# Kernel tuning notes

Hardware: AMD Instinct MI355X
Metric: run time of the kernel (lower is better)

Reference implementation:

```python
import jax, jax.numpy as jnp
import numpy as np

M, N, EMB, H, ENC, T = 4096, 256, 64, 128, 128, 100


def _lstm_dir(x, Wih, Whh, b, h0, c0):
    # x: (T, M, E); PyTorch LSTM gate order i, f, g, o
    def step(carry, xt):
        h, c = carry
        g = xt @ Wih + h @ Whh + b
        i, f, gg, o = jnp.split(g, 4, axis=-1)
        c = jax.nn.sigmoid(f) * c + jax.nn.sigmoid(i) * jnp.tanh(gg)
        h = jax.nn.sigmoid(o) * jnp.tanh(c)
        return (h, c), h
    _, hs = jax.lax.scan(step, (h0, c0), x)
    return hs  # (T, M, H)


def setup_inputs() -> dict:
    key = jax.random.key(0)
    ks = jax.random.split(key, 14)
    rn = lambda k, sh, s: jax.random.normal(k, sh, jnp.float32) * s
    return {
        "lane_features": jax.random.normal(ks[0], (M, 600), jnp.float32),
        "obs_encoding": jax.random.normal(ks[1], (N, 128), jnp.float32),
        "embed_W": rn(ks[2], (4, EMB), 0.5),
        "embed_b": jnp.zeros((EMB,), jnp.float32),
        "attn_W": rn(ks[3], (128, 100), 0.09),
        "attn_b": jnp.zeros((100,), jnp.float32),
        "Wih_f": rn(ks[4], (EMB, 4 * H), 0.08),
        "Whh_f": rn(ks[5], (H, 4 * H), 0.08),
        "b_f": jnp.zeros((4 * H,), jnp.float32),
        "Wih_b": rn(ks[6], (EMB, 4 * H), 0.08),
        "Whh_b": rn(ks[7], (H, 4 * H), 0.08),
        "b_b": jnp.zeros((4 * H,), jnp.float32),
        "h0": rn(ks[8], (2, 1, H), 0.1),
        "c0": rn(ks[9], (2, 1, H), 0.1),
        "enc_W": rn(ks[10], (8 * H, ENC), 0.03),
        "enc_b": jnp.zeros((ENC,), jnp.float32),
        "same_obs_mask": jax.random.randint(ks[11], (M, 1), 0, N, jnp.int32),
    }


def reference(lane_features, obs_encoding, embed_W, embed_b, attn_W, attn_b,
              Wih_f, Whh_f, b_f, Wih_b, Whh_b, b_b, h0, c0, enc_W, enc_b,
              same_obs_mask):
    Mloc = lane_features.shape[0]
    E = embed_W.shape[1]
    Hh = Whh_f.shape[0]
    # last 400 features -> 100 timesteps x 4 features, then embed + relu
    feat = lane_features[:, -400:].reshape(Mloc * 100, 4)
    lane_embed = jax.nn.relu(feat @ embed_W + embed_b).reshape(Mloc, 100, E)
    # per-obstacle attention over the 100 lane points
    scores = jax.nn.softmax(jax.nn.relu(obs_encoding @ attn_W + attn_b), axis=1)  # (N, 100)
    # the original per-obs_id scatter loop == a single gather by obstacle id
    att = scores[same_obs_mask[:, 0]]  # (M, 100)
    x = jnp.transpose(lane_embed, (1, 0, 2))  # (T, M, E)
    h0f = jnp.broadcast_to(h0[0], (Mloc, Hh)); c0f = jnp.broadcast_to(c0[0], (Mloc, Hh))
    h0b = jnp.broadcast_to(h0[1], (Mloc, Hh)); c0b = jnp.broadcast_to(c0[1], (Mloc, Hh))
    hs_f = _lstm_dir(x, Wih_f, Whh_f, b_f, h0f, c0f)
    hs_b = _lstm_dir(x[::-1], Wih_b, Whh_b, b_b, h0b, c0b)[::-1]
    ls = jnp.transpose(jnp.concatenate([hs_f, hs_b], axis=-1), (1, 0, 2))  # (M, T, 2H)
    front = ls[:, 0, :]
    back = ls[:, -1, :]
    mx = jnp.max(ls, axis=1)
    attn_states = jnp.sum(ls * att[:, :, None], axis=1)
    out = jnp.concatenate([front, back, mx, attn_states], axis=1)  # (M, 8H)
    return jax.nn.relu(out @ enc_W + enc_b)
```

## Files before the change

### kernel.cpp

```cpp
#include <hip/hip_runtime.h>
#include <hip/hip_bf16.h>

#define MROWS 4096
#define TSTEPS 100
#define EMB 64
#define HID 128
#define GATES 512
#define KTOT 192
#define ROWS_PB 32
#define SROW 200

typedef _Float16 half8 __attribute__((ext_vector_type(8)));
typedef _Float16 half4v __attribute__((ext_vector_type(4)));
typedef float f32x4 __attribute__((ext_vector_type(4)));

#define LOG2E  1.44269504f
#define LOG2E2 2.88539008f

__device__ __forceinline__ float rcpf(float x) { return __builtin_amdgcn_rcpf(x); }
__device__ __forceinline__ float ex2(float x) { return __builtin_amdgcn_exp2f(x); }

__global__ void attn_scores_kernel(const float* __restrict__ obs,
                                   const float* __restrict__ attn_W,
                                   const float* __restrict__ attn_b,
                                   float* __restrict__ scores) {
    const int row = blockIdx.x;
    const int tid = threadIdx.x;
    __shared__ float obs_s[128];
    __shared__ float red[128];

    obs_s[tid] = obs[row * 128 + tid];
    __syncthreads();

    float s = -1e30f;
    if (tid < 100) {
        float a = attn_b[tid];
        #pragma unroll 4
        for (int k = 0; k < 128; k++) a += obs_s[k] * attn_W[k * 100 + tid];
        s = fmaxf(a, 0.f);
    }
    red[tid] = s;
    __syncthreads();
    for (int off = 64; off > 0; off >>= 1) {
        if (tid < off) red[tid] = fmaxf(red[tid], red[tid + off]);
        __syncthreads();
    }
    const float m = red[0];
    __syncthreads();
    const float e = (tid < 100) ? __expf(s - m) : 0.f;
    red[tid] = e;
    __syncthreads();
    for (int off = 64; off > 0; off >>= 1) {
        if (tid < off) red[tid] += red[tid + off];
        __syncthreads();
    }
    const float inv = __fdividef(1.f, red[0]);
    if (tid < 100) scores[row * 100 + tid] = e * inv;
}

__global__ void encw_prep_kernel(const float* __restrict__ enc_W,
                                 _Float16* __restrict__ encWT) {
    __shared__ float tile[64][129];
    const int k0 = blockIdx.x * 64;
    const int tid = threadIdx.x;
    #pragma unroll
    for (int i = 0; i < 32; i++) {
        const int idx = tid + i * 256;
        const int rr = idx >> 7, cc = idx & 127;
        tile[rr][cc] = enc_W[(k0 + rr) * 128 + cc];
    }
    __syncthreads();
    const int c = tid >> 1, hh = tid & 1;
    #pragma unroll
    for (int j = 0; j < 32; j++) {
        encWT[c * 1024 + k0 + hh * 32 + j] = (_Float16)tile[hh * 32 + j][c];
    }
}

__launch_bounds__(512, 2)
__global__ void lstm_kernel(const float* __restrict__ lane_features,
                            const float* __restrict__ embed_W,
                            const float* __restrict__ embed_b,
                            const float* __restrict__ Wih_f,
                            const float* __restrict__ Whh_f,
                            const float* __restrict__ b_f,
                            const float* __restrict__ Wih_b,
                            const float* __restrict__ Whh_b,
                            const float* __restrict__ b_b,
                            const float* __restrict__ h0,
                            const float* __restrict__ c0,
                            const int*   __restrict__ mask,
                            const float* __restrict__ scores,
                            float* __restrict__ out_feat) {
    const int blk = blockIdx.x;
    const int d = blk >> 7;
    const int rowbase = (blk & 127) * ROWS_PB;
    const int tid = threadIdx.x;
    const int wave = tid >> 6;
    const int lane = tid & 63;
    const int lane16 = lane & 15;
    const int quad = lane >> 4;

    const float* Wih = d ? Wih_b : Wih_f;
    const float* Whh = d ? Whh_b : Whh_f;
    const float* bia = d ? b_b : b_f;

    __shared__ __attribute__((aligned(16))) _Float16 panel[2][ROWS_PB][SROW];
    __shared__ float att_s[ROWS_PB][100];

    const int erow = tid >> 4;
    const int cc = (tid & 15) * 4;
    float ew_r[4][4], eb_r[4];
    #pragma unroll
    for (int j = 0; j < 4; j++) {
        #pragma unroll
        for (int jj = 0; jj < 4; jj++) ew_r[j][jj] = embed_W[j * EMB + cc + jj];
    }
    #pragma unroll
    for (int jj = 0; jj < 4; jj++) eb_r[jj] = embed_b[cc + jj];

    {
        const int r = tid >> 4, tcol = tid & 15;
        const int mr = mask[rowbase + r];
        for (int t = tcol; t < 100; t += 16) att_s[r][t] = scores[mr * 100 + t];
    }

    const int unitg = wave * 16 + lane16;
    half8 Bf[24];
    #pragma unroll
    for (int ct = 0; ct < 4; ct++) {
        const float scale = (ct == 2) ? LOG2E2 : LOG2E;
        const int col = ct * 128 + unitg;
        #pragma unroll
        for (int ki = 0; ki < 6; ki++) {
            half8 b;
            #pragma unroll
            for (int j = 0; j < 8; j++) {
                const int kk = ki * 32 + quad * 8 + j;
                const float w = (kk < EMB) ? Wih[kk * GATES + col]
                                           : Whh[(kk - EMB) * GATES + col];
                b[j] = (_Float16)(w * scale);
            }
            Bf[ct * 6 + ki] = b;
        }
    }
    float bgate[4];
    #pragma unroll
    for (int ct = 0; ct < 4; ct++)
        bgate[ct] = bia[ct * 128 + unitg] * ((ct == 2) ? LOG2E2 : LOG2E);

    float cst[8], mx[8], as[8], h0s[8], hl[8];
    const float cinit = c0[d * 128 + unitg];
    #pragma unroll
    for (int p = 0; p < 8; p++) {
        cst[p] = cinit; mx[p] = -1e30f; as[p] = 0.f; h0s[p] = 0.f; hl[p] = 0.f;
    }

    for (int idx = tid; idx < ROWS_PB * HID; idx += 512) {
        const int r = idx >> 7, u = idx & 127;
        panel[0][r][EMB + u] = (_Float16)h0[d * 128 + u];
    }

    {
        const int t0 = d ? (TSTEPS - 1) : 0;
        const float4 fv = *(const float4*)(lane_features + (long)(rowbase + erow) * 600 + 200 + 4 * t0);
        #pragma unroll
        for (int jj = 0; jj < 4; jj++) {
            float e = eb_r[jj] + fv.x * ew_r[0][jj] + fv.y * ew_r[1][jj]
                               + fv.z * ew_r[2][jj] + fv.w * ew_r[3][jj];
            panel[0][erow][cc + jj] = (_Float16)fmaxf(e, 0.f);
        }
    }
    __syncthreads();

    for (int s = 0; s < TSTEPS; s++) {
        const int p = s & 1;
        const int t = d ? (TSTEPS - 1 - s) : s;

        float4 fv;
        if (s < TSTEPS - 1) {
            const int tn = d ? (TSTEPS - 2 - s) : (s + 1);
            fv = *(const float4*)(lane_features + (long)(rowbase + erow) * 600 + 200 + 4 * tn);
        }

        float aw[8];
        #pragma unroll
        for (int pp = 0; pp < 8; pp++) {
            const int row_local = (pp >> 2) * 16 + quad * 4 + (pp & 3);
            aw[pp] = att_s[row_local][t];
        }

        f32x4 acc[2][4];
        #pragma unroll
        for (int rt = 0; rt < 2; rt++)
            #pragma unroll
            for (int ct = 0; ct < 4; ct++) {
                const float bg = bgate[ct];
                acc[rt][ct] = (f32x4){bg, bg, bg, bg};
            }

        #pragma unroll
        for (int ki = 0; ki < 6; ki++) {
            const half8 a0 = *(const half8*)&panel[p][lane16][ki * 32 + quad * 8];
            const half8 a1 = *(const half8*)&panel[p][16 + lane16][ki * 32 + quad * 8];
            #pragma unroll
            for (int ct = 0; ct < 4; ct++) {
                acc[0][ct] = __builtin_amdgcn_mfma_f32_16x16x32_f16(a0, Bf[ct * 6 + ki], acc[0][ct], 0, 0, 0);
                acc[1][ct] = __builtin_amdgcn_mfma_f32_16x16x32_f16(a1, Bf[ct * 6 + ki], acc[1][ct], 0, 0, 0);
            }
        }

        #pragma unroll
        for (int rt = 0; rt < 2; rt++) {
            #pragma unroll
            for (int r = 0; r < 4; r++) {
                const int pp = rt * 4 + r;
                const int row_local = rt * 16 + quad * 4 + r;
                const float gi = acc[rt][0][r];
                const float gf = acc[rt][1][r];
                const float gg = fminf(acc[rt][2][r], 80.f);
                const float go = acc[rt][3][r];
                const float Ei = ex2(-gi);
                const float Ef = ex2(-gf);
                const float Eg = ex2(gg);
                const float Eo = ex2(-go);
                const float sf = rcpf(1.f + Ef);
                const float r1 = rcpf((1.f + Ei) * (Eg + 1.f));
                const float cn = sf * cst[pp] + (Eg - 1.f) * r1;
                const float Ec = ex2(fminf(cn * LOG2E2, 80.f));
                const float r2 = rcpf((1.f + Eo) * (Ec + 1.f));
                const float h = (Ec - 1.f) * r2;
                cst[pp] = cn;
                hl[pp] = h;
                mx[pp] = fmaxf(mx[pp], h);
                as[pp] = fmaf(aw[pp], h, as[pp]);
                panel[1 - p][row_local][EMB + unitg] = (_Float16)h;
            }
        }
        if (s == 0) {
            #pragma unroll
            for (int pp = 0; pp < 8; pp++) h0s[pp] = hl[pp];
        }

        if (s < TSTEPS - 1) {
            float e0 = eb_r[0] + fv.x * ew_r[0][0] + fv.y * ew_r[1][0] + fv.z * ew_r[2][0] + fv.w * ew_r[3][0];
            float e1 = eb_r[1] + fv.x * ew_r[0][1] + fv.y * ew_r[1][1] + fv.z * ew_r[2][1] + fv.w * ew_r[3][1];
            float e2 = eb_r[2] + fv.x * ew_r[0][2] + fv.y * ew_r[1][2] + fv.z * ew_r[2][2] + fv.w * ew_r[3][2];
            float e3 = eb_r[3] + fv.x * ew_r[0][3] + fv.y * ew_r[1][3] + fv.z * ew_r[2][3] + fv.w * ew_r[3][3];
            panel[1 - p][erow][cc]     = (_Float16)fmaxf(e0, 0.f);
            panel[1 - p][erow][cc + 1] = (_Float16)fmaxf(e1, 0.f);
            panel[1 - p][erow][cc + 2] = (_Float16)fmaxf(e2, 0.f);
            panel[1 - p][erow][cc + 3] = (_Float16)fmaxf(e3, 0.f);
        }
        __syncthreads();
    }

    #pragma unroll
    for (int pp = 0; pp < 8; pp++) {
        const int row_local = (pp >> 2) * 16 + quad * 4 + (pp & 3);
        const long ro = (long)(rowbase + row_local) * 1024;
        const int cu = d * 128 + unitg;
        const float fr = d ? hl[pp] : h0s[pp];
        const float bk = d ? h0s[pp] : hl[pp];
        out_feat[ro + cu]       = fr;
        out_feat[ro + 256 + cu] = bk;
        out_feat[ro + 512 + cu] = mx[pp];
        out_feat[ro + 768 + cu] = as[pp];
    }
}

__launch_bounds__(256, 2)
__global__ void enc_kernel(const float* __restrict__ out_feat,
                           const _Float16* __restrict__ encWT,
                           const float* __restrict__ enc_b,
                           float* __restrict__ out) {
    const int rb = blockIdx.x * 16;
    const int tid = threadIdx.x;
    const int wave = tid >> 6;
    const int lane = tid & 63;
    const int lane16 = lane & 15;
    const int quad = lane >> 4;

    __shared__ __attribute__((aligned(16))) _Float16 A16[16][1032];

    #pragma unroll
    for (int i = 0; i < 16; i++) {
        const int u = tid + i * 256;
        const int row = u >> 8, kc = u & 255;
        const float4 v = *(const float4*)(out_feat + (long)(rb + row) * 1024 + kc * 4);
        half4v hv;
        hv[0] = (_Float16)v.x; hv[1] = (_Float16)v.y;
        hv[2] = (_Float16)v.z; hv[3] = (_Float16)v.w;
        *(half4v*)&A16[row][kc * 4] = hv;
    }
    __syncthreads();

    const int col0 = wave * 32 + lane16;
    f32x4 acc0 = {0.f, 0.f, 0.f, 0.f}, acc1 = {0.f, 0.f, 0.f, 0.f};

    #pragma unroll 4
    for (int it = 0; it < 32; it++) {
        const half8 a  = *(const half8*)&A16[lane16][it * 32 + quad * 8];
        const half8 b0 = *(const half8*)(encWT + (long)col0 * 1024 + it * 32 + quad * 8);
        const half8 b1 = *(const half8*)(encWT + (long)(col0 + 16) * 1024 + it * 32 + quad * 8);
        acc0 = __builtin_amdgcn_mfma_f32_16x16x32_f16(a, b0, acc0, 0, 0, 0);
        acc1 = __builtin_amdgcn_mfma_f32_16x16x32_f16(a, b1, acc1, 0, 0, 0);
    }

    const float bb0 = enc_b[col0], bb1 = enc_b[col0 + 16];
    #pragma unroll
    for (int r = 0; r < 4; r++) {
        const int row = rb + quad * 4 + r;
        out[(long)row * 128 + col0]      = fmaxf(acc0[r] + bb0, 0.f);
        out[(long)row * 128 + col0 + 16] = fmaxf(acc1[r] + bb1, 0.f);
    }
}

extern "C" void kernel_launch(void* const* d_in, const int* in_sizes, int n_in,
                              void* d_out, int out_size, void* d_ws, size_t ws_size,
                              hipStream_t stream) {
    const float* lane_features = (const float*)d_in[0];
    const float* obs_encoding  = (const float*)d_in[1];
    const float* embed_W = (const float*)d_in[2];
    const float* embed_b = (const float*)d_in[3];
    const float* attn_W  = (const float*)d_in[4];
    const float* attn_b  = (const float*)d_in[5];
    const float* Wih_f   = (const float*)d_in[6];
    const float* Whh_f   = (const float*)d_in[7];
    const float* b_f     = (const float*)d_in[8];
    const float* Wih_b   = (const float*)d_in[9];
    const float* Whh_b   = (const float*)d_in[10];
    const float* b_b     = (const float*)d_in[11];
    const float* h0      = (const float*)d_in[12];
    const float* c0      = (const float*)d_in[13];
    const float* enc_W   = (const float*)d_in[14];
    const float* enc_b   = (const float*)d_in[15];
    const int*   mask    = (const int*)d_in[16];

    float*     scores   = (float*)d_ws;
    _Float16*  encWT    = (_Float16*)((char*)d_ws + (128 << 10));
    float*     out_feat = (float*)((char*)d_ws + (384 << 10));
    float*     out      = (float*)d_out;

    attn_scores_kernel<<<256, 128, 0, stream>>>(obs_encoding, attn_W, attn_b, scores);
    encw_prep_kernel<<<16, 256, 0, stream>>>(enc_W, encWT);
    lstm_kernel<<<256, 512, 0, stream>>>(lane_features, embed_W, embed_b,
                                         Wih_f, Whh_f, b_f, Wih_b, Whh_b, b_b,
                                         h0, c0, mask, scores, out_feat);
    enc_kernel<<<256, 256, 0, stream>>>(out_feat, encWT, enc_b, out);
}
```

Before: 305.7 us.

## Merge prep kernels, store intermediate features as fp16, pre-swizzle encoder weights

Combines the attention-score and encoder-weight prep into one launch, removing a kernel launch. The LSTM kernel now writes its pooled features in fp16, halving the intermediate buffer traffic, and the encoder kernel loads them with 16-byte copies and no conversion. Encoder weights are pre-arranged into per-lane MFMA fragment order so each B-operand load is contiguous across the wavefront. The fp16 feature storage rounds the features before the GEMM, though the GEMM already converted them to fp16 before.

```diff
diff --git a/kernel.cpp b/kernel.cpp
--- a/kernel.cpp
+++ b/kernel.cpp
@@ -11,7 +11,6 @@
 #define SROW 200
 
 typedef _Float16 half8 __attribute__((ext_vector_type(8)));
-typedef _Float16 half4v __attribute__((ext_vector_type(4)));
 typedef float f32x4 __attribute__((ext_vector_type(4)));
 
 #define LOG2E  1.44269504f
@@ -20,60 +19,61 @@
 __device__ __forceinline__ float rcpf(float x) { return __builtin_amdgcn_rcpf(x); }
 __device__ __forceinline__ float ex2(float x) { return __builtin_amdgcn_exp2f(x); }
 
-__global__ void attn_scores_kernel(const float* __restrict__ obs,
-                                   const float* __restrict__ attn_W,
-                                   const float* __restrict__ attn_b,
-                                   float* __restrict__ scores) {
-    const int row = blockIdx.x;
+__global__ void prep_kernel(const float* __restrict__ obs,
+                            const float* __restrict__ attn_W,
+                            const float* __restrict__ attn_b,
+                            float* __restrict__ scores,
+                            const float* __restrict__ enc_W,
+                            _Float16* __restrict__ frag) {
     const int tid = threadIdx.x;
-    __shared__ float obs_s[128];
-    __shared__ float red[128];
-
-    obs_s[tid] = obs[row * 128 + tid];
-    __syncthreads();
-
-    float s = -1e30f;
-    if (tid < 100) {
-        float a = attn_b[tid];
-        #pragma unroll 4
-        for (int k = 0; k < 128; k++) a += obs_s[k] * attn_W[k * 100 + tid];
-        s = fmaxf(a, 0.f);
-    }
-    red[tid] = s;
-    __syncthreads();
-    for (int off = 64; off > 0; off >>= 1) {
-        if (tid < off) red[tid] = fmaxf(red[tid], red[tid + off]);
-        __syncthreads();
-    }
-    const float m = red[0];
-    __syncthreads();
-    const float e = (tid < 100) ? __expf(s - m) : 0.f;
-    red[tid] = e;
-    __syncthreads();
-    for (int off = 64; off > 0; off >>= 1) {
-        if (tid < off) red[tid] += red[tid + off];
-        __syncthreads();
-    }
-    const float inv = __fdividef(1.f, red[0]);
-    if (tid < 100) scores[row * 100 + tid] = e * inv;
-}
-
-__global__ void encw_prep_kernel(const float* __restrict__ enc_W,
-                                 _Float16* __restrict__ encWT) {
-    __shared__ float tile[64][129];
-    const int k0 = blockIdx.x * 64;
-    const int tid = threadIdx.x;
-    #pragma unroll
-    for (int i = 0; i < 32; i++) {
-        const int idx = tid + i * 256;
-        const int rr = idx >> 7, cc = idx & 127;
-        tile[rr][cc] = enc_W[(k0 + rr) * 128 + cc];
-    }
-    __syncthreads();
-    const int c = tid >> 1, hh = tid & 1;
-    #pragma unroll
-    for (int j = 0; j < 32; j++) {
-        encWT[c * 1024 + k0 + hh * 32 + j] = (_Float16)tile[hh * 32 + j][c];
+    if (blockIdx.x < 256) {
+        const int row = blockIdx.x;
+        __shared__ float obs_s[128];
+        __shared__ float red[128];
+
+        if (tid < 128) obs_s[tid] = obs[row * 128 + tid];
+        __syncthreads();
+
+        float s = -1e30f;
+        if (tid < 100) {
+            float a = attn_b[tid];
+            #pragma unroll 4
+            for (int k = 0; k < 128; k++) a += obs_s[k] * attn_W[k * 100 + tid];
+            s = fmaxf(a, 0.f);
+        }
+        if (tid < 128) red[tid] = s;
+        __syncthreads();
+        for (int off = 64; off > 0; off >>= 1) {
+            if (tid < off) red[tid] = fmaxf(red[tid], red[tid + off]);
+            __syncthreads();
+        }
+        const float m = red[0];
+        __syncthreads();
+        const float e = (tid < 100) ? __expf(s - m) : 0.f;
+        if (tid < 128) red[tid] = e;
+        __syncthreads();
+        for (int off = 64; off > 0; off >>= 1) {
+            if (tid < off) red[tid] += red[tid + off];
+            __syncthreads();
+        }
+        const float inv = __fdividef(1.f, red[0]);
+        if (tid < 100) scores[row * 100 + tid] = e * inv;
+    } else {
+        const int pb = blockIdx.x - 256;
+        const int pair = pb * 16 + (tid >> 4);
+        const int tile = pair >> 5;
+        const int it   = pair & 31;
+        const int sub  = tid & 15;
+        #pragma unroll
+        for (int li = 0; li < 4; li++) {
+            const int l = sub * 4 + li;
+            const int c = tile * 16 + (l & 15);
+            const int kbase = it * 32 + (l >> 4) * 8;
+            half8 v;
+            #pragma unroll
+            for (int j = 0; j < 8; j++) v[j] = (_Float16)enc_W[(kbase + j) * 128 + c];
+            *(half8*)(frag + (((long)(tile * 32 + it)) * 64 + l) * 8) = v;
+        }
     }
 }
 
@@ -91,7 +91,7 @@
                             const float* __restrict__ c0,
                             const int*   __restrict__ mask,
                             const float* __restrict__ scores,
-                            float* __restrict__ out_feat) {
+                            _Float16* __restrict__ out_feat) {
     const int blk = blockIdx.x;
     const int d = blk >> 7;
     const int rowbase = (blk & 127) * ROWS_PB;
@@ -262,16 +262,16 @@
         const int cu = d * 128 + unitg;
         const float fr = d ? hl[pp] : h0s[pp];
         const float bk = d ? h0s[pp] : hl[pp];
-        out_feat[ro + cu]       = fr;
-        out_feat[ro + 256 + cu] = bk;
-        out_feat[ro + 512 + cu] = mx[pp];
-        out_feat[ro + 768 + cu] = as[pp];
+        out_feat[ro + cu]       = (_Float16)fr;
+        out_feat[ro + 256 + cu] = (_Float16)bk;
+        out_feat[ro + 512 + cu] = (_Float16)mx[pp];
+        out_feat[ro + 768 + cu] = (_Float16)as[pp];
     }
 }
 
 __launch_bounds__(256, 2)
-__global__ void enc_kernel(const float* __restrict__ out_feat,
-                           const _Float16* __restrict__ encWT,
+__global__ void enc_kernel(const _Float16* __restrict__ out_feat,
+                           const _Float16* __restrict__ frag,
                            const float* __restrict__ enc_b,
                            float* __restrict__ out) {
     const int rb = blockIdx.x * 16;
@@ -284,25 +284,24 @@
     __shared__ __attribute__((aligned(16))) _Float16 A16[16][1032];
 
     #pragma unroll
-    for (int i = 0; i < 16; i++) {
+    for (int i = 0; i < 8; i++) {
         const int u = tid + i * 256;
-        const int row = u >> 8, kc = u & 255;
-        const float4 v = *(const float4*)(out_feat + (long)(rb + row) * 1024 + kc * 4);
-        half4v hv;
-        hv[0] = (_Float16)v.x; hv[1] = (_Float16)v.y;
-        hv[2] = (_Float16)v.z; hv[3] = (_Float16)v.w;
-        *(half4v*)&A16[row][kc * 4] = hv;
+        const int row = u >> 7, kc = u & 127;
+        *(half8*)&A16[row][kc * 8] = *(const half8*)(out_feat + (long)(rb + row) * 1024 + kc * 8);
     }
     __syncthreads();
 
     const int col0 = wave * 32 + lane16;
     f32x4 acc0 = {0.f, 0.f, 0.f, 0.f}, acc1 = {0.f, 0.f, 0.f, 0.f};
+
+    const _Float16* f0 = frag + ((long)(2 * wave) * 32 * 64) * 8 + lane * 8;
+    const _Float16* f1 = frag + ((long)(2 * wave + 1) * 32 * 64) * 8 + lane * 8;
 
     #pragma unroll 4
     for (int it = 0; it < 32; it++) {
         const half8 a  = *(const half8*)&A16[lane16][it * 32 + quad * 8];
-        const half8 b0 = *(const half8*)(encWT + (long)col0 * 1024 + it * 32 + quad * 8);
-        const half8 b1 = *(const half8*)(encWT + (long)(col0 + 16) * 1024 + it * 32 + quad * 8);
+        const half8 b0 = *(const half8*)(f0 + (long)it * 64 * 8);
+        const half8 b1 = *(const half8*)(f1 + (long)it * 64 * 8);
         acc0 = __builtin_amdgcn_mfma_f32_16x16x32_f16(a, b0, acc0, 0, 0, 0);
         acc1 = __builtin_amdgcn_mfma_f32_16x16x32_f16(a, b1, acc1, 0, 0, 0);
     }
@@ -338,14 +337,14 @@
     const int*   mask    = (const int*)d_in[16];
 
     float*     scores   = (float*)d_ws;
-    _Float16*  encWT    = (_Float16*)((char*)d_ws + (128 << 10));
-    float*     out_feat = (float*)((char*)d_ws + (384 << 10));
+    _Float16*  frag     = (_Float16*)((char*)d_ws + (128 << 10));
+    _Float16*  out_feat = (_Float16*)((char*)d_ws + (512 << 10));
     float*     out      = (float*)d_out;
 
-    attn_scores_kernel<<<256, 128, 0, stream>>>(obs_encoding, attn_W, attn_b, scores);
-    encw_prep_kernel<<<16, 256, 0, stream>>>(enc_W, encWT);
+    prep_kernel<<<272, 256, 0, stream>>>(obs_encoding, attn_W, attn_b, scores,
+                                         enc_W, frag);
     lstm_kernel<<<256, 512, 0, stream>>>(lane_features, embed_W, embed_b,
                                          Wih_f, Whh_f, b_f, Wih_b, Whh_b, b_b,
                                          h0, c0, mask, scores, out_feat);
-    enc_kernel<<<256, 256, 0, stream>>>(out_feat, encWT, enc_b, out);
+    enc_kernel<<<256, 256, 0, stream>>>(out_feat, frag, enc_b, out);
 }
```

New measurement: 299.6 us. 2.0% less time.
